# Kernel tuning notes

Measured on AMD Instinct MI355X. Metric: run time of the kernel, lower is better.

## Reference

```python
import jax, jax.numpy as jnp
import numpy as np

# Locally-connected 2D convolution (torch legacy SpatialConvolutionLocal)
# out[b,o,h,w] = sum_{c,i,j} weight[h,w,o,c,i,j] * x_pad[b,c,h*dH+i,w*dW+j] + bias[o,h,w]

B, CIN, IH, IW = 32, 32, 64, 64
COUT, KH, KW = 64, 3, 3
DH, DW = 1, 1
PADH, PADW = 1, 1
OH = (IH + 2 * PADH - KH) // DH + 1
OW = (IW + 2 * PADW - KW) // DW + 1


def setup_inputs() -> dict:
    key = jax.random.key(0)
    k1, k2, k3 = jax.random.split(key, 3)
    stdv = 1.0 / np.sqrt(KW * KH * CIN)
    x = jax.random.normal(k1, (B, CIN, IH, IW), dtype=jnp.float32)
    weight = jax.random.uniform(k2, (OH, OW, COUT, CIN, KH, KW), dtype=jnp.float32,
                                minval=-stdv, maxval=stdv)
    bias = jax.random.uniform(k3, (COUT, OH, OW), dtype=jnp.float32,
                              minval=-stdv, maxval=stdv)
    return {"x": x, "weight": weight, "bias": bias}


def _extract_patches(x):
    # x: [B, C, IH, IW] -> patches [B, C, KH, KW, OH, OW]
    xp = jnp.pad(x, ((0, 0), (0, 0), (PADH, PADH), (PADW, PADW)))
    rows = []
    for i in range(KH):  # small fixed kernel loop (9 iters), not a data-dim loop
        cols = []
        for j in range(KW):
            cols.append(xp[:, :, i:i + OH * DH:DH, j:j + OW * DW:DW])
        rows.append(jnp.stack(cols, axis=2))  # [B, C, KW, OH, OW]
    return jnp.stack(rows, axis=2)  # [B, C, KH, KW, OH, OW]


def reference(x, weight, bias):
    patches = _extract_patches(x)  # [B, C, KH, KW, OH, OW]
    # per-position GEMM: distinct weight matrix at each (h, w)
    out = jnp.einsum('bcijhw,hwocij->bohw', patches, weight)
    return out + bias[None]  # [B, COUT, OH, OW]
```

## Files before the change

### kernel.cpp

```cpp
#include <hip/hip_runtime.h>


#define KP 88
#define NPOS 4

typedef __attribute__((ext_vector_type(8))) short short8;
typedef __attribute__((ext_vector_type(16))) float f32x16;

__device__ __forceinline__ unsigned f2bf(float f) {
    unsigned u = __builtin_bit_cast(unsigned, f);
    return (u + 0x7FFFu + ((u >> 16) & 1u)) >> 16;
}

__global__ __launch_bounds__(256) void lcconv_kernel(
    const float* __restrict__ xg,
    const float* __restrict__ wg,
    const float* __restrict__ bg,
    float* __restrict__ outg)
{
    __shared__ unsigned short Wl[NPOS * 32 * KP];
    __shared__ unsigned short Pl[NPOS * 32 * KP];

    const int tid = threadIdx.x;
    const int bid = blockIdx.x;
    const int oh = bid & 1;
    const int ws = (bid >> 1) & 15;
    const int h  = bid >> 5;
    const int w0 = ws * 4;
    const int og = oh * 32;

    {
        unsigned short* base = (tid & 128) ? Pl : Wl;
        int row = tid & 127;
        *(short8*)(base + row * KP + 72) = (short8)0;
    }

    f32x16 acc;
#pragma unroll
    for (int i = 0; i < 16; i++) acc[i] = 0.f;

    const int lane = tid & 63;
    const int wv   = tid >> 6;
    const int mrow = lane & 31;
    const int g    = lane >> 5;

    for (int cc = 0; cc < 4; cc++) {
        const int c0 = cc * 8;
        __syncthreads();

#pragma unroll
        for (int it = 0; it < 9; it++) {
            int f4 = it * 256 + tid;
            int run = f4 / 18;
            int within = f4 - run * 18;
            int p = run >> 5, o = run & 31;
            const float4 w4 = *(const float4*)(
                wg + ((h * 64 + (w0 + p)) * 64 + og + o) * 288 + c0 * 9 + within * 4);
            unsigned long long pk = (unsigned long long)f2bf(w4.x)
                | ((unsigned long long)f2bf(w4.y) << 16)
                | ((unsigned long long)f2bf(w4.z) << 32)
                | ((unsigned long long)f2bf(w4.w) << 48);
            *(unsigned long long*)(Wl + (p * 32 + o) * KP + within * 4) = pk;
        }

#pragma unroll
        for (int it = 0; it < 18; it++) {
            int pr = it * 256 + tid;
            int e = pr * 2;
            int p = e / 2304;
            int rem = e - p * 2304;
            int b = rem / 72;
            int k = rem - b * 72;
            unsigned pk = 0;
#pragma unroll
            for (int half = 0; half < 2; half++) {
                int kk = k + half;
                int c  = kk / 9;
                int r9 = kk - c * 9;
                int i3 = r9 / 3;
                int j  = r9 - i3 * 3;
                int y  = h + i3 - 1;
                int xx = w0 + p + j - 1;
                float v = (y >= 0 && y < 64 && xx >= 0 && xx < 64)
                        ? xg[((b * 32 + c0 + c) * 64 + y) * 64 + xx] : 0.f;
                pk |= f2bf(v) << (16 * half);
            }
            *(unsigned*)(Pl + (p * 32 + b) * KP + k) = pk;
        }
        __syncthreads();

#pragma unroll
        for (int ks = 0; ks < 5; ks++) {
            short8 a  = *(const short8*)(Pl + (wv * 32 + mrow) * KP + ks * 16 + g * 8);
            short8 b8 = *(const short8*)(Wl + (wv * 32 + mrow) * KP + ks * 16 + g * 8);
            acc = __builtin_amdgcn_mfma_f32_32x32x16_bf16(a, b8, acc, 0, 0, 0);
        }
    }
    __syncthreads();

    float* outl = (float*)Wl;
#pragma unroll
    for (int r = 0; r < 16; r++) {
        int row = (r & 3) + 8 * (r >> 2) + 4 * g;
        outl[(wv * 32 + row) * 32 + mrow] = acc[r];
    }
    __syncthreads();

#pragma unroll
    for (int it = 0; it < 4; it++) {
        int id = it * 256 + tid;
        int b = id >> 5;
        int o = id & 31;
        float4 v;
        v.x = outl[0 * 1024 + b * 32 + o];
        v.y = outl[1 * 1024 + b * 32 + o];
        v.z = outl[2 * 1024 + b * 32 + o];
        v.w = outl[3 * 1024 + b * 32 + o];
        const float4 bb = *(const float4*)(bg + ((og + o) * 64 + h) * 64 + w0);
        v.x += bb.x; v.y += bb.y; v.z += bb.z; v.w += bb.w;
        *(float4*)(outg + ((b * 64 + og + o) * 64 + h) * 64 + w0) = v;
    }
}

extern "C" void kernel_launch(void* const* d_in, const int* in_sizes, int n_in,
                              void* d_out, int out_size, void* d_ws, size_t ws_size,
                              hipStream_t stream) {
    const float* x = (const float*)d_in[0];
    const float* w = (const float*)d_in[1];
    const float* b = (const float*)d_in[2];
    float* out = (float*)d_out;
    lcconv_kernel<<<dim3(2048), dim3(256), 0, stream>>>(x, w, b, out);
}
```

Before: 547.4 us.

## Prefetch next channel chunk into registers and load input rows as vectorized float2

```diff
diff --git a/kernel.cpp b/kernel.cpp
--- a/kernel.cpp
+++ b/kernel.cpp
@@ -2,7 +2,6 @@
 
 
 #define KP 88
-#define NPOS 4
 
 typedef __attribute__((ext_vector_type(8))) short short8;
 typedef __attribute__((ext_vector_type(16))) float f32x16;
@@ -12,14 +11,14 @@
     return (u + 0x7FFFu + ((u >> 16) & 1u)) >> 16;
 }
 
-__global__ __launch_bounds__(256) void lcconv_kernel(
+__global__ __launch_bounds__(256, 3) void lcconv_kernel(
     const float* __restrict__ xg,
     const float* __restrict__ wg,
     const float* __restrict__ bg,
     float* __restrict__ outg)
 {
-    __shared__ unsigned short Wl[NPOS * 32 * KP];
-    __shared__ unsigned short Pl[NPOS * 32 * KP];
+    __shared__ unsigned short Wl[4 * 32 * KP];
+    __shared__ unsigned short Pl[4 * 32 * KP];
 
     const int tid = threadIdx.x;
     const int bid = blockIdx.x;
@@ -44,50 +43,94 @@
     const int mrow = lane & 31;
     const int g    = lane >> 5;
 
+    float4 wreg[9];
+    float2 xreg[12];
+
+#pragma unroll
+    for (int it = 0; it < 9; it++) {
+        int f4 = it * 256 + tid;
+        int run = f4 / 18, within = f4 - run * 18;
+        int p = run >> 5, o = run & 31;
+        wreg[it] = *(const float4*)(
+            wg + ((h * 64 + (w0 + p)) * 64 + og + o) * 288 + within * 4);
+    }
+#pragma unroll
+    for (int it = 0; it < 12; it++) {
+        int task = it * 256 + tid;
+        int f2i = task & 3, row = task >> 2;
+        int b = row / 24, rem = row - b * 24;
+        int c = rem / 3, y3 = rem - c * 3;
+        int y = h + y3 - 1;
+        int gx0 = w0 - 2 + 2 * f2i;
+        if ((unsigned)y < 64u && (unsigned)gx0 < 64u)
+            xreg[it] = *(const float2*)(xg + ((b * 32 + c) * 64 + y) * 64 + gx0);
+        else
+            xreg[it] = float2{0.f, 0.f};
+    }
+
     for (int cc = 0; cc < 4; cc++) {
-        const int c0 = cc * 8;
         __syncthreads();
 
 #pragma unroll
         for (int it = 0; it < 9; it++) {
             int f4 = it * 256 + tid;
-            int run = f4 / 18;
-            int within = f4 - run * 18;
-            int p = run >> 5, o = run & 31;
-            const float4 w4 = *(const float4*)(
-                wg + ((h * 64 + (w0 + p)) * 64 + og + o) * 288 + c0 * 9 + within * 4);
+            int run = f4 / 18, within = f4 - run * 18;
+            float4 w4 = wreg[it];
             unsigned long long pk = (unsigned long long)f2bf(w4.x)
                 | ((unsigned long long)f2bf(w4.y) << 16)
                 | ((unsigned long long)f2bf(w4.z) << 32)
                 | ((unsigned long long)f2bf(w4.w) << 48);
-            *(unsigned long long*)(Wl + (p * 32 + o) * KP + within * 4) = pk;
+            *(unsigned long long*)(Wl + run * KP + within * 4) = pk;
         }
 
 #pragma unroll
-        for (int it = 0; it < 18; it++) {
-            int pr = it * 256 + tid;
-            int e = pr * 2;
-            int p = e / 2304;
-            int rem = e - p * 2304;
-            int b = rem / 72;
-            int k = rem - b * 72;
-            unsigned pk = 0;
+        for (int it = 0; it < 12; it++) {
+            int task = it * 256 + tid;
+            int f2i = task & 3, row = task >> 2;
+            int b = row / 24, rem = row - b * 24;
+            int c = rem / 3, y3 = rem - c * 3;
+            int kb = c * 9 + y3 * 3;
+            int pb = b * KP + kb;
+            unsigned bx0 = f2bf(xreg[it].x);
+            unsigned bx1 = f2bf(xreg[it].y);
 #pragma unroll
-            for (int half = 0; half < 2; half++) {
-                int kk = k + half;
-                int c  = kk / 9;
-                int r9 = kk - c * 9;
-                int i3 = r9 / 3;
-                int j  = r9 - i3 * 3;
-                int y  = h + i3 - 1;
-                int xx = w0 + p + j - 1;
-                float v = (y >= 0 && y < 64 && xx >= 0 && xx < 64)
-                        ? xg[((b * 32 + c0 + c) * 64 + y) * 64 + xx] : 0.f;
-                pk |= f2bf(v) << (16 * half);
+            for (int q = 0; q < 2; q++) {
+                int xc = f2i * 2 + q;
+                unsigned short bv = (unsigned short)(q ? bx1 : bx0);
+#pragma unroll
+                for (int j = 0; j < 3; j++) {
+                    int p = xc - 1 - j;
+                    if ((unsigned)p < 4u)
+                        Pl[p * (32 * KP) + pb + j] = bv;
+                }
             }
-            *(unsigned*)(Pl + (p * 32 + b) * KP + k) = pk;
         }
         __syncthreads();
+
+        if (cc < 3) {
+            const int c0n = (cc + 1) * 8;
+#pragma unroll
+            for (int it = 0; it < 9; it++) {
+                int f4 = it * 256 + tid;
+                int run = f4 / 18, within = f4 - run * 18;
+                int p = run >> 5, o = run & 31;
+                wreg[it] = *(const float4*)(
+                    wg + ((h * 64 + (w0 + p)) * 64 + og + o) * 288 + c0n * 9 + within * 4);
+            }
+#pragma unroll
+            for (int it = 0; it < 12; it++) {
+                int task = it * 256 + tid;
+                int f2i = task & 3, row = task >> 2;
+                int b = row / 24, rem = row - b * 24;
+                int c = rem / 3, y3 = rem - c * 3;
+                int y = h + y3 - 1;
+                int gx0 = w0 - 2 + 2 * f2i;
+                if ((unsigned)y < 64u && (unsigned)gx0 < 64u)
+                    xreg[it] = *(const float2*)(xg + ((b * 32 + c0n + c) * 64 + y) * 64 + gx0);
+                else
+                    xreg[it] = float2{0.f, 0.f};
+            }
+        }
 
 #pragma unroll
         for (int ks = 0; ks < 5; ks++) {
```

After: 510.8 us. -6.7%, faster.
